# Performance work log

Hardware: AMD Instinct MI355X
Metric: run time of the kernel (lower is better)

Reference implementation:

```python
import jax, jax.numpy as jnp
import numpy as np


def setup_inputs() -> dict:
    key = jax.random.key(0)
    ks = jax.random.split(key, 13)
    T, B, E, H = 2048, 32, 512, 512
    stdv = 1.0 / np.sqrt(H)
    u = lambda k, shape: jax.random.uniform(k, shape, jnp.float32, -stdv, stdv)
    return {
        "embeds": jax.random.normal(ks[0], (T, B, E), jnp.float32),
        "h_0": jnp.zeros((B, H), jnp.float32),
        "c_0": jnp.zeros((B, H), jnp.float32),
        "W_gx": u(ks[1], (E, H)), "W_gh": u(ks[2], (H, H)), "b_g": u(ks[3], (H,)),
        "W_ix": u(ks[4], (E, H)), "W_ih": u(ks[5], (H, H)), "b_i": u(ks[6], (H,)),
        "W_fx": u(ks[7], (E, H)), "W_fh": u(ks[8], (H, H)), "b_f": u(ks[9], (H,)),
        "W_ox": u(ks[10], (E, H)), "W_oh": u(ks[11], (H, H)), "b_o": u(ks[12], (H,)),
    }


def reference(embeds, h_0, c_0, W_gx, W_gh, b_g, W_ix, W_ih, b_i,
              W_fx, W_fh, b_f, W_ox, W_oh, b_o):
    # Fuse the 4 input-side GEMMs into one [T,B,E]@[E,4H] (no recurrence dep).
    Wx = jnp.concatenate([W_gx, W_ix, W_fx, W_ox], axis=1)   # [E, 4H]
    Wh = jnp.concatenate([W_gh, W_ih, W_fh, W_oh], axis=1)   # [H, 4H]
    b = jnp.concatenate([b_g, b_i, b_f, b_o], axis=0)        # [4H]
    H = h_0.shape[-1]
    x_gates = embeds @ Wx + b                                 # [T, B, 4H]

    def step(carry, xg):
        h, c = carry
        gates = xg + h @ Wh                                   # [B, 4H]
        g, i, f, o = jnp.split(gates, 4, axis=-1)
        g = jnp.tanh(g)
        i = jax.nn.sigmoid(i)
        f = jax.nn.sigmoid(f)
        o = jax.nn.sigmoid(o)
        c = g * i + c * f
        h = jnp.tanh(c) * o
        return (h, c), h

    (h_T, c_T), seq = jax.lax.scan(step, (h_0, c_0), x_gates)
    return seq, h_T, c_T
```

## Files before the change

kernel.cpp:

```cpp
#include <hip/hip_runtime.h>


#define T_STEPS 2048
#define BATCH   32
#define EDIM    512
#define HDIM    512
#define NW      128
#define NJ      4
#define NCOL    16
#define WG_THREADS 128
#define BSTRIDE 1032

typedef unsigned int       u32;
typedef unsigned long long u64;
typedef unsigned short     u16;
typedef float  floatx4 __attribute__((ext_vector_type(4)));
typedef __bf16 bf16x8  __attribute__((ext_vector_type(8)));

union BF16U { __bf16 b; u16 u; };

__device__ __forceinline__ u16 f2bf(float f) { BF16U x; x.b = (__bf16)f; return x.u; }

__device__ __forceinline__ float fast_sigmoid(float x) {
  return 1.0f / (1.0f + __expf(-x));
}
__device__ __forceinline__ float fast_tanh(float x) {
  float e = __expf(-2.0f * fabsf(x));
  float t = (1.0f - e) / (1.0f + e);
  return x >= 0.0f ? t : -t;
}

__global__ void lstm_prep(const float* __restrict__ emb, u16* __restrict__ embb,
                          const float* __restrict__ h0, u16* __restrict__ hb0,
                          u32* __restrict__ flags) {
  const size_t n4 = (size_t)T_STEPS * BATCH * EDIM / 4;
  size_t stride = (size_t)gridDim.x * blockDim.x;
  size_t gid = (size_t)blockIdx.x * blockDim.x + threadIdx.x;
  for (size_t i = gid; i < n4; i += stride) {
    float4 v = ((const float4*)emb)[i];
    ushort4 o;
    o.x = f2bf(v.x); o.y = f2bf(v.y); o.z = f2bf(v.z); o.w = f2bf(v.w);
    ((ushort4*)embb)[i] = o;
  }
  if (gid < (size_t)BATCH * HDIM) hb0[gid] = f2bf(h0[gid]);
  if (gid < NW) flags[gid] = 0u;
}

__global__ void __launch_bounds__(WG_THREADS)
lstm_rec(const u16* __restrict__ embb,
         const float* __restrict__ c0,
         const float* __restrict__ Wx0, const float* __restrict__ Wh0, const float* __restrict__ b0,
         const float* __restrict__ Wx1, const float* __restrict__ Wh1, const float* __restrict__ b1,
         const float* __restrict__ Wx2, const float* __restrict__ Wh2, const float* __restrict__ b2,
         const float* __restrict__ Wx3, const float* __restrict__ Wh3, const float* __restrict__ b3,
         u16* __restrict__ hbuf,
         u32* __restrict__ flags,
         float* __restrict__ out) {
  __shared__ __align__(16) __bf16 Blds[NCOL][BSTRIDE];
  __shared__ __align__(16) float wbuf[2][NCOL][20];

  const int tid    = threadIdx.x;
  const int w      = blockIdx.x;
  const int j0     = w * NJ;
  const int lane   = tid & 63;
  const int waveid = tid >> 6;
  const int nlo    = lane & 15;
  const int q      = lane >> 4;
  const int mrow   = waveid * 16 + nlo;

  const float* Wx[4] = {Wx0, Wx1, Wx2, Wx3};
  const float* Wh[4] = {Wh0, Wh1, Wh2, Wh3};

  for (int g = 0; g < 4; ++g) {
    for (int base = 0; base < EDIM; base += WG_THREADS) {
      int kk = base + tid;
      float4 wx = *(const float4*)(Wx[g] + (size_t)kk * HDIM + j0);
      float4 wh = *(const float4*)(Wh[g] + (size_t)kk * HDIM + j0);
      Blds[g*NJ+0][kk] = (__bf16)wx.x;  Blds[g*NJ+0][EDIM+kk] = (__bf16)wh.x;
      Blds[g*NJ+1][kk] = (__bf16)wx.y;  Blds[g*NJ+1][EDIM+kk] = (__bf16)wh.y;
      Blds[g*NJ+2][kk] = (__bf16)wx.z;  Blds[g*NJ+2][EDIM+kk] = (__bf16)wh.z;
      Blds[g*NJ+3][kk] = (__bf16)wx.w;  Blds[g*NJ+3][EDIM+kk] = (__bf16)wh.w;
    }
  }

  const int r0 = nlo >> 2;
  const int ej = nlo & 3;
  const int er = waveid * 16 + q * 4 + r0;
  const int jg = j0 + ej;
  float cst = c0[(size_t)er * HDIM + jg];
  const float bgv = b0[jg], biv = b1[jg], bfv = b2[jg], bov = b3[jg];

  __syncthreads();

  const u64* f8 = (const u64*)flags;

  for (int t = 0; t < T_STEPS; ++t) {
    floatx4 acc0 = {0.f, 0.f, 0.f, 0.f};
    floatx4 acc1 = {0.f, 0.f, 0.f, 0.f};
    const u16* erow = embb + ((size_t)t * BATCH + mrow) * EDIM;
#pragma unroll
    for (int s = 0; s < 16; s += 2) {
      int k0 = s * 32 + q * 8;
      int k1 = (s + 1) * 32 + q * 8;
      bf16x8 a0 = *reinterpret_cast<const bf16x8*>(erow + k0);
      bf16x8 a1 = *reinterpret_cast<const bf16x8*>(erow + k1);
      bf16x8 w0 = *reinterpret_cast<const bf16x8*>(&Blds[nlo][k0]);
      bf16x8 w1 = *reinterpret_cast<const bf16x8*>(&Blds[nlo][k1]);
      acc0 = __builtin_amdgcn_mfma_f32_16x16x32_bf16(a0, w0, acc0, 0, 0, 0);
      acc1 = __builtin_amdgcn_mfma_f32_16x16x32_bf16(a1, w1, acc1, 0, 0, 0);
    }

    for (;;) {
      u64 v = __hip_atomic_load(&f8[lane], __ATOMIC_RELAXED, __HIP_MEMORY_SCOPE_AGENT);
      int ok = ((u32)v >= (u32)t) && ((u32)(v >> 32) >= (u32)t);
      if (__all(ok)) break;
      __builtin_amdgcn_s_sleep(1);
    }

    const u16* hcur  = hbuf + (size_t)(t & 1) * (BATCH * HDIM);
    u16*       hnext = hbuf + (size_t)((t + 1) & 1) * (BATCH * HDIM);

    const u64* hrow = (const u64*)(hcur + (size_t)mrow * HDIM);
#pragma unroll
    for (int s = 0; s < 16; s += 2) {
      int k0 = s * 32 + q * 8;
      int k1 = (s + 1) * 32 + q * 8;
      union { u64 qv[2]; bf16x8 v; } ua, ub;
      ua.qv[0] = __hip_atomic_load(&hrow[(k0 >> 2) + 0], __ATOMIC_RELAXED, __HIP_MEMORY_SCOPE_AGENT);
      ua.qv[1] = __hip_atomic_load(&hrow[(k0 >> 2) + 1], __ATOMIC_RELAXED, __HIP_MEMORY_SCOPE_AGENT);
      ub.qv[0] = __hip_atomic_load(&hrow[(k1 >> 2) + 0], __ATOMIC_RELAXED, __HIP_MEMORY_SCOPE_AGENT);
      ub.qv[1] = __hip_atomic_load(&hrow[(k1 >> 2) + 1], __ATOMIC_RELAXED, __HIP_MEMORY_SCOPE_AGENT);
      bf16x8 w0 = *reinterpret_cast<const bf16x8*>(&Blds[nlo][EDIM + k0]);
      bf16x8 w1 = *reinterpret_cast<const bf16x8*>(&Blds[nlo][EDIM + k1]);
      acc0 = __builtin_amdgcn_mfma_f32_16x16x32_bf16(ua.v, w0, acc0, 0, 0, 0);
      acc1 = __builtin_amdgcn_mfma_f32_16x16x32_bf16(ub.v, w1, acc1, 0, 0, 0);
    }

    floatx4 sum;
#pragma unroll
    for (int r = 0; r < 4; ++r) sum[r] = acc0[r] + acc1[r];
    *reinterpret_cast<floatx4*>(&wbuf[waveid][nlo][q * 4]) = sum;

    float pg = wbuf[waveid][ej     ][q * 4 + r0];
    float pi = wbuf[waveid][ej +  4][q * 4 + r0];
    float pf = wbuf[waveid][ej +  8][q * 4 + r0];
    float po = wbuf[waveid][ej + 12][q * 4 + r0];

    float gv = fast_tanh   (pg + bgv);
    float iv = fast_sigmoid(pi + biv);
    float fv = fast_sigmoid(pf + bfv);
    float ov = fast_sigmoid(po + bov);
    cst = gv * iv + cst * fv;
    float hv = fast_tanh(cst) * ov;

    __hip_atomic_store(hnext + (size_t)er * HDIM + jg, f2bf(hv),
                       __ATOMIC_RELAXED, __HIP_MEMORY_SCOPE_AGENT);
    __syncthreads();
    if (tid == 0)
      __hip_atomic_store(&flags[w], (u32)(t + 1),
                         __ATOMIC_RELAXED, __HIP_MEMORY_SCOPE_AGENT);

    out[((size_t)t * BATCH + er) * HDIM + jg] = hv;
    if (t == T_STEPS - 1) {
      const size_t seqN = (size_t)T_STEPS * BATCH * HDIM;
      out[seqN + (size_t)er * HDIM + jg] = hv;
      out[seqN + (size_t)BATCH * HDIM + (size_t)er * HDIM + jg] = cst;
    }
  }
}

extern "C" void kernel_launch(void* const* d_in, const int* in_sizes, int n_in,
                              void* d_out, int out_size, void* d_ws, size_t ws_size,
                              hipStream_t stream) {
  const float* emb = (const float*)d_in[0];
  const float* h0  = (const float*)d_in[1];
  const float* c0  = (const float*)d_in[2];
  const float* Wgx = (const float*)d_in[3];
  const float* Wgh = (const float*)d_in[4];
  const float* bg  = (const float*)d_in[5];
  const float* Wix = (const float*)d_in[6];
  const float* Wih = (const float*)d_in[7];
  const float* bi  = (const float*)d_in[8];
  const float* Wfx = (const float*)d_in[9];
  const float* Wfh = (const float*)d_in[10];
  const float* bf  = (const float*)d_in[11];
  const float* Wox = (const float*)d_in[12];
  const float* Woh = (const float*)d_in[13];
  const float* bo  = (const float*)d_in[14];
  float* out = (float*)d_out;

  char* ws = (char*)d_ws;
  const size_t embb_bytes = (size_t)T_STEPS * BATCH * EDIM * 2;
  u16* embb  = (u16*)ws;
  u16* hbuf  = (u16*)(ws + embb_bytes);
  u32* flags = (u32*)(ws + embb_bytes + 2 * (size_t)BATCH * HDIM * 2);

  lstm_prep<<<4096, 256, 0, stream>>>(emb, embb, h0, hbuf, flags);
  lstm_rec<<<NW, WG_THREADS, 0, stream>>>(embb, c0,
                                          Wgx, Wgh, bg,
                                          Wix, Wih, bi,
                                          Wfx, Wfh, bf,
                                          Wox, Woh, bo,
                                          hbuf, flags, out);
}
```

Baseline: 7.516 ms.

## Consolidate recurrent LSTM into 32 large workgroups to cut cross-WG sync cost

Reshapes the persistent recurrent kernel from 128 workgroups of 2 waves (4 hidden columns each) into 32 workgroups of 8 waves (16 hidden columns each). Each wave now covers one of 2 batch tiles and one of 4 column tiles. Weights move to dynamic LDS of about 142KB per workgroup. The per-step flag poll only has to check 32 producers, using 16 lanes. The aim is to shrink the per-timestep grid-wide barrier and flag-polling latency. The cost is fewer CUs active and more waves contending for LDS and MFMA units on each CU.

```diff
diff --git a/kernel.cpp b/kernel.cpp
--- a/kernel.cpp
+++ b/kernel.cpp
@@ -5,10 +5,10 @@
 #define BATCH   32
 #define EDIM    512
 #define HDIM    512
-#define NW      128
-#define NJ      4
-#define NCOL    16
-#define WG_THREADS 128
+#define NW      32
+#define NJH     16
+#define NCOL    64
+#define WG_THREADS 512
 #define BSTRIDE 1032
 
 typedef unsigned int       u32;
@@ -16,6 +16,10 @@
 typedef unsigned short     u16;
 typedef float  floatx4 __attribute__((ext_vector_type(4)));
 typedef __bf16 bf16x8  __attribute__((ext_vector_type(8)));
+
+#define BLDS_BYTES (NCOL * BSTRIDE * 2)
+#define WBUF_OFF   BLDS_BYTES
+#define LDS_BYTES  (BLDS_BYTES + 8 * 16 * 20 * 4)
 
 union BF16U { __bf16 b; u16 u; };
 
@@ -56,37 +60,44 @@
          u16* __restrict__ hbuf,
          u32* __restrict__ flags,
          float* __restrict__ out) {
-  __shared__ __align__(16) __bf16 Blds[NCOL][BSTRIDE];
-  __shared__ __align__(16) float wbuf[2][NCOL][20];
+  extern __shared__ __align__(16) char dynlds[];
+  __bf16 (*Blds)[BSTRIDE] = (__bf16(*)[BSTRIDE])dynlds;
+  float  (*wbuf)[16][20]  = (float(*)[16][20])(dynlds + WBUF_OFF);
 
   const int tid    = threadIdx.x;
   const int w      = blockIdx.x;
-  const int j0     = w * NJ;
+  const int j0     = w * NJH;
   const int lane   = tid & 63;
   const int waveid = tid >> 6;
+  const int mtile  = waveid & 1;
+  const int ntile  = waveid >> 1;
   const int nlo    = lane & 15;
   const int q      = lane >> 4;
-  const int mrow   = waveid * 16 + nlo;
+  const int mrow   = mtile * 16 + nlo;
+  const int pbase  = ntile * 16;
 
   const float* Wx[4] = {Wx0, Wx1, Wx2, Wx3};
   const float* Wh[4] = {Wh0, Wh1, Wh2, Wh3};
 
-  for (int g = 0; g < 4; ++g) {
-    for (int base = 0; base < EDIM; base += WG_THREADS) {
-      int kk = base + tid;
-      float4 wx = *(const float4*)(Wx[g] + (size_t)kk * HDIM + j0);
-      float4 wh = *(const float4*)(Wh[g] + (size_t)kk * HDIM + j0);
-      Blds[g*NJ+0][kk] = (__bf16)wx.x;  Blds[g*NJ+0][EDIM+kk] = (__bf16)wh.x;
-      Blds[g*NJ+1][kk] = (__bf16)wx.y;  Blds[g*NJ+1][EDIM+kk] = (__bf16)wh.y;
-      Blds[g*NJ+2][kk] = (__bf16)wx.z;  Blds[g*NJ+2][EDIM+kk] = (__bf16)wh.z;
-      Blds[g*NJ+3][kk] = (__bf16)wx.w;  Blds[g*NJ+3][EDIM+kk] = (__bf16)wh.w;
+  {
+    const int kk = tid;
+    for (int g = 0; g < 4; ++g) {
+      for (int cq = 0; cq < 4; ++cq) {
+        const float4 wxv = *(const float4*)(Wx[g] + (size_t)kk * HDIM + j0 + cq * 4);
+        const float4 whv = *(const float4*)(Wh[g] + (size_t)kk * HDIM + j0 + cq * 4);
+        const int p = cq * 16 + g * 4;
+        Blds[p + 0][kk] = (__bf16)wxv.x;  Blds[p + 0][EDIM + kk] = (__bf16)whv.x;
+        Blds[p + 1][kk] = (__bf16)wxv.y;  Blds[p + 1][EDIM + kk] = (__bf16)whv.y;
+        Blds[p + 2][kk] = (__bf16)wxv.z;  Blds[p + 2][EDIM + kk] = (__bf16)whv.z;
+        Blds[p + 3][kk] = (__bf16)wxv.w;  Blds[p + 3][EDIM + kk] = (__bf16)whv.w;
+      }
     }
   }
 
   const int r0 = nlo >> 2;
   const int ej = nlo & 3;
-  const int er = waveid * 16 + q * 4 + r0;
-  const int jg = j0 + ej;
+  const int er = mtile * 16 + q * 4 + r0;
+  const int jg = j0 + ntile * 4 + ej;
   float cst = c0[(size_t)er * HDIM + jg];
   const float bgv = b0[jg], biv = b1[jg], bfv = b2[jg], bov = b3[jg];
 
@@ -104,15 +115,18 @@
       int k1 = (s + 1) * 32 + q * 8;
       bf16x8 a0 = *reinterpret_cast<const bf16x8*>(erow + k0);
       bf16x8 a1 = *reinterpret_cast<const bf16x8*>(erow + k1);
-      bf16x8 w0 = *reinterpret_cast<const bf16x8*>(&Blds[nlo][k0]);
-      bf16x8 w1 = *reinterpret_cast<const bf16x8*>(&Blds[nlo][k1]);
+      bf16x8 w0 = *reinterpret_cast<const bf16x8*>(&Blds[pbase + nlo][k0]);
+      bf16x8 w1 = *reinterpret_cast<const bf16x8*>(&Blds[pbase + nlo][k1]);
       acc0 = __builtin_amdgcn_mfma_f32_16x16x32_bf16(a0, w0, acc0, 0, 0, 0);
       acc1 = __builtin_amdgcn_mfma_f32_16x16x32_bf16(a1, w1, acc1, 0, 0, 0);
     }
 
     for (;;) {
-      u64 v = __hip_atomic_load(&f8[lane], __ATOMIC_RELAXED, __HIP_MEMORY_SCOPE_AGENT);
-      int ok = ((u32)v >= (u32)t) && ((u32)(v >> 32) >= (u32)t);
+      int ok = 1;
+      if (lane < 16) {
+        u64 v = __hip_atomic_load(&f8[lane], __ATOMIC_RELAXED, __HIP_MEMORY_SCOPE_AGENT);
+        ok = ((u32)v >= (u32)t) && ((u32)(v >> 32) >= (u32)t);
+      }
       if (__all(ok)) break;
       __builtin_amdgcn_s_sleep(1);
     }
@@ -130,8 +144,8 @@
       ua.qv[1] = __hip_atomic_load(&hrow[(k0 >> 2) + 1], __ATOMIC_RELAXED, __HIP_MEMORY_SCOPE_AGENT);
       ub.qv[0] = __hip_atomic_load(&hrow[(k1 >> 2) + 0], __ATOMIC_RELAXED, __HIP_MEMORY_SCOPE_AGENT);
       ub.qv[1] = __hip_atomic_load(&hrow[(k1 >> 2) + 1], __ATOMIC_RELAXED, __HIP_MEMORY_SCOPE_AGENT);
-      bf16x8 w0 = *reinterpret_cast<const bf16x8*>(&Blds[nlo][EDIM + k0]);
-      bf16x8 w1 = *reinterpret_cast<const bf16x8*>(&Blds[nlo][EDIM + k1]);
+      bf16x8 w0 = *reinterpret_cast<const bf16x8*>(&Blds[pbase + nlo][EDIM + k0]);
+      bf16x8 w1 = *reinterpret_cast<const bf16x8*>(&Blds[pbase + nlo][EDIM + k1]);
       acc0 = __builtin_amdgcn_mfma_f32_16x16x32_bf16(ua.v, w0, acc0, 0, 0, 0);
       acc1 = __builtin_amdgcn_mfma_f32_16x16x32_bf16(ub.v, w1, acc1, 0, 0, 0);
     }
@@ -195,11 +209,18 @@
   u16* hbuf  = (u16*)(ws + embb_bytes);
   u32* flags = (u32*)(ws + embb_bytes + 2 * (size_t)BATCH * HDIM * 2);
 
+  static int lds_attr_set = 0;
+  if (!lds_attr_set) {
+    hipFuncSetAttribute(reinterpret_cast<const void*>(lstm_rec),
+                        hipFuncAttributeMaxDynamicSharedMemorySize, LDS_BYTES);
+    lds_attr_set = 1;
+  }
+
   lstm_prep<<<4096, 256, 0, stream>>>(emb, embb, h0, hbuf, flags);
-  lstm_rec<<<NW, WG_THREADS, 0, stream>>>(embb, c0,
-                                          Wgx, Wgh, bg,
-                                          Wix, Wih, bi,
-                                          Wfx, Wfh, bf,
-                                          Wox, Woh, bo,
-                                          hbuf, flags, out);
-}
+  lstm_rec<<<NW, WG_THREADS, LDS_BYTES, stream>>>(embb, c0,
+                                                  Wgx, Wgh, bg,
+                                                  Wix, Wih, bi,
+                                                  Wfx, Wfh, bf,
+                                                  Wox, Woh, bo,
+                                                  hbuf, flags, out);
+}
```

New measurement: 22.86 ms. +204.2%, slower.

## Replace per-block flag barrier with sentinel-tagged triple-buffered hidden state

Applied to the files above, without the earlier changes.

Removes the separate per-workgroup flag array and the __syncthreads plus flag publish each step. Consumers instead spin directly on the hidden-state data, treating a NaN-pattern sentinel as not ready, and reuse the loaded values for the recurrent MFMA. A third h buffer lets each block reset the buffer two steps ahead to the sentinel. Hidden outputs are packed into 64-bit stores, one per row per block, through a small shared-memory transpose. This shortens the critical path between steps, but relies on a real h quad never equalling the sentinel and on the ordering from an explicit vmcnt wait.

```diff
diff --git a/kernel.cpp b/kernel.cpp
--- a/kernel.cpp
+++ b/kernel.cpp
@@ -10,6 +10,7 @@
 #define NCOL    16
 #define WG_THREADS 128
 #define BSTRIDE 1032
+#define HQ      (BATCH * HDIM / 4)
 
 typedef unsigned int       u32;
 typedef unsigned long long u64;
@@ -17,6 +18,8 @@
 typedef float  floatx4 __attribute__((ext_vector_type(4)));
 typedef __bf16 bf16x8  __attribute__((ext_vector_type(8)));
 
+#define SENT64 0x7FC07FC07FC07FC0ULL
+
 union BF16U { __bf16 b; u16 u; };
 
 __device__ __forceinline__ u16 f2bf(float f) { BF16U x; x.b = (__bf16)f; return x.u; }
@@ -31,8 +34,7 @@
 }
 
 __global__ void lstm_prep(const float* __restrict__ emb, u16* __restrict__ embb,
-                          const float* __restrict__ h0, u16* __restrict__ hb0,
-                          u32* __restrict__ flags) {
+                          const float* __restrict__ h0, u16* __restrict__ hb) {
   const size_t n4 = (size_t)T_STEPS * BATCH * EDIM / 4;
   size_t stride = (size_t)gridDim.x * blockDim.x;
   size_t gid = (size_t)blockIdx.x * blockDim.x + threadIdx.x;
@@ -42,8 +44,9 @@
     o.x = f2bf(v.x); o.y = f2bf(v.y); o.z = f2bf(v.z); o.w = f2bf(v.w);
     ((ushort4*)embb)[i] = o;
   }
-  if (gid < (size_t)BATCH * HDIM) hb0[gid] = f2bf(h0[gid]);
-  if (gid < NW) flags[gid] = 0u;
+  if (gid < (size_t)BATCH * HDIM) hb[gid] = f2bf(h0[gid]);
+  u64* hq = (u64*)(hb + (size_t)BATCH * HDIM);
+  if (gid < 2 * HQ) hq[gid] = SENT64;
 }
 
 __global__ void __launch_bounds__(WG_THREADS)
@@ -54,10 +57,10 @@
          const float* __restrict__ Wx2, const float* __restrict__ Wh2, const float* __restrict__ b2,
          const float* __restrict__ Wx3, const float* __restrict__ Wh3, const float* __restrict__ b3,
          u16* __restrict__ hbuf,
-         u32* __restrict__ flags,
          float* __restrict__ out) {
   __shared__ __align__(16) __bf16 Blds[NCOL][BSTRIDE];
   __shared__ __align__(16) float wbuf[2][NCOL][20];
+  __shared__ __align__(16) float pbuf[2][16][4];
 
   const int tid    = threadIdx.x;
   const int w      = blockIdx.x;
@@ -90,9 +93,13 @@
   float cst = c0[(size_t)er * HDIM + jg];
   const float bgv = b0[jg], biv = b1[jg], bfv = b2[jg], bov = b3[jg];
 
+  const bool publane = (lane < 16);
+  const int  pubrow  = waveid * 16 + nlo;
+  const size_t puboff = (((size_t)pubrow * HDIM + j0) >> 2);
+
   __syncthreads();
 
-  const u64* f8 = (const u64*)flags;
+  u64* const hq = (u64*)hbuf;
 
   for (int t = 0; t < T_STEPS; ++t) {
     floatx4 acc0 = {0.f, 0.f, 0.f, 0.f};
@@ -110,26 +117,34 @@
       acc1 = __builtin_amdgcn_mfma_f32_16x16x32_bf16(a1, w1, acc1, 0, 0, 0);
     }
 
+    const u64* hc = hq + (size_t)(t % 3) * HQ;
+    u64*       hn = hq + (size_t)((t + 1) % 3) * HQ;
+    u64*       hs = hq + (size_t)((t + 2) % 3) * HQ;
+
+    const u64* hrow = hc + (size_t)mrow * (HDIM / 4);
+    u64 hreg[32];
     for (;;) {
-      u64 v = __hip_atomic_load(&f8[lane], __ATOMIC_RELAXED, __HIP_MEMORY_SCOPE_AGENT);
-      int ok = ((u32)v >= (u32)t) && ((u32)(v >> 32) >= (u32)t);
+      bool ok = true;
+#pragma unroll
+      for (int i = 0; i < 16; ++i) {
+        int base = i * 8 + q * 2;
+        hreg[2*i]   = __hip_atomic_load(&hrow[base],   __ATOMIC_RELAXED, __HIP_MEMORY_SCOPE_AGENT);
+        hreg[2*i+1] = __hip_atomic_load(&hrow[base+1], __ATOMIC_RELAXED, __HIP_MEMORY_SCOPE_AGENT);
+        ok = ok && (hreg[2*i] != SENT64) && (hreg[2*i+1] != SENT64);
+      }
       if (__all(ok)) break;
-      __builtin_amdgcn_s_sleep(1);
-    }
-
-    const u16* hcur  = hbuf + (size_t)(t & 1) * (BATCH * HDIM);
-    u16*       hnext = hbuf + (size_t)((t + 1) & 1) * (BATCH * HDIM);
-
-    const u64* hrow = (const u64*)(hcur + (size_t)mrow * HDIM);
+    }
+
+    if (publane)
+      __hip_atomic_store(&hs[puboff], SENT64, __ATOMIC_RELAXED, __HIP_MEMORY_SCOPE_AGENT);
+
 #pragma unroll
     for (int s = 0; s < 16; s += 2) {
       int k0 = s * 32 + q * 8;
       int k1 = (s + 1) * 32 + q * 8;
       union { u64 qv[2]; bf16x8 v; } ua, ub;
-      ua.qv[0] = __hip_atomic_load(&hrow[(k0 >> 2) + 0], __ATOMIC_RELAXED, __HIP_MEMORY_SCOPE_AGENT);
-      ua.qv[1] = __hip_atomic_load(&hrow[(k0 >> 2) + 1], __ATOMIC_RELAXED, __HIP_MEMORY_SCOPE_AGENT);
-      ub.qv[0] = __hip_atomic_load(&hrow[(k1 >> 2) + 0], __ATOMIC_RELAXED, __HIP_MEMORY_SCOPE_AGENT);
-      ub.qv[1] = __hip_atomic_load(&hrow[(k1 >> 2) + 1], __ATOMIC_RELAXED, __HIP_MEMORY_SCOPE_AGENT);
+      ua.qv[0] = hreg[2*s];     ua.qv[1] = hreg[2*s+1];
+      ub.qv[0] = hreg[2*s+2];   ub.qv[1] = hreg[2*s+3];
       bf16x8 w0 = *reinterpret_cast<const bf16x8*>(&Blds[nlo][EDIM + k0]);
       bf16x8 w1 = *reinterpret_cast<const bf16x8*>(&Blds[nlo][EDIM + k1]);
       acc0 = __builtin_amdgcn_mfma_f32_16x16x32_bf16(ua.v, w0, acc0, 0, 0, 0);
@@ -153,17 +168,24 @@
     cst = gv * iv + cst * fv;
     float hv = fast_tanh(cst) * ov;
 
-    __hip_atomic_store(hnext + (size_t)er * HDIM + jg, f2bf(hv),
-                       __ATOMIC_RELAXED, __HIP_MEMORY_SCOPE_AGENT);
-    __syncthreads();
-    if (tid == 0)
-      __hip_atomic_store(&flags[w], (u32)(t + 1),
-                         __ATOMIC_RELAXED, __HIP_MEMORY_SCOPE_AGENT);
-
-    out[((size_t)t * BATCH + er) * HDIM + jg] = hv;
+    pbuf[waveid][q * 4 + r0][ej] = hv;
+
+    float4 hv4;
+    if (publane) {
+      floatx4 v4 = *reinterpret_cast<floatx4*>(&pbuf[waveid][nlo][0]);
+      hv4.x = v4[0]; hv4.y = v4[1]; hv4.z = v4[2]; hv4.w = v4[3];
+    }
+    asm volatile("s_waitcnt vmcnt(0)" ::: "memory");
+    if (publane) {
+      u64 pk = (u64)f2bf(hv4.x) | ((u64)f2bf(hv4.y) << 16)
+             | ((u64)f2bf(hv4.z) << 32) | ((u64)f2bf(hv4.w) << 48);
+      __hip_atomic_store(&hn[puboff], pk, __ATOMIC_RELAXED, __HIP_MEMORY_SCOPE_AGENT);
+      *reinterpret_cast<float4*>(out + ((size_t)t * BATCH + pubrow) * HDIM + j0) = hv4;
+    }
     if (t == T_STEPS - 1) {
       const size_t seqN = (size_t)T_STEPS * BATCH * HDIM;
-      out[seqN + (size_t)er * HDIM + jg] = hv;
+      if (publane)
+        *reinterpret_cast<float4*>(out + seqN + (size_t)pubrow * HDIM + j0) = hv4;
       out[seqN + (size_t)BATCH * HDIM + (size_t)er * HDIM + jg] = cst;
     }
   }
@@ -193,13 +215,12 @@
   const size_t embb_bytes = (size_t)T_STEPS * BATCH * EDIM * 2;
   u16* embb  = (u16*)ws;
   u16* hbuf  = (u16*)(ws + embb_bytes);
-  u32* flags = (u32*)(ws + embb_bytes + 2 * (size_t)BATCH * HDIM * 2);
-
-  lstm_prep<<<4096, 256, 0, stream>>>(emb, embb, h0, hbuf, flags);
+
+  lstm_prep<<<4096, 256, 0, stream>>>(emb, embb, h0, hbuf);
   lstm_rec<<<NW, WG_THREADS, 0, stream>>>(embb, c0,
                                           Wgx, Wgh, bg,
                                           Wix, Wih, bi,
                                           Wfx, Wfh, bf,
                                           Wox, Woh, bo,
-                                          hbuf, flags, out);
-}
+                                          hbuf, out);
+}
```

Result: slower. 10.75 ms (+43.0%).

## Use per-wave flags, packed h stores, and prefetch embeddings into registers

Applied to the files above, without the earlier changes.

Splits the step-completion flags so each wave publishes and waits on its own set, which removes the per-step block-wide __syncthreads. Each group of four lanes packs its bf16 h values into one 64-bit atomic store and writes the fp32 output as a float4. The next step's embedding rows are prefetched into registers while the current step runs, and the sleep in the spin loop is removed. The costs are higher register pressure, busier spinning on the flags, and reliance on a raw s_waitcnt to order the h store before the flag store.

```diff
diff --git a/kernel.cpp b/kernel.cpp
--- a/kernel.cpp
+++ b/kernel.cpp
@@ -31,7 +31,7 @@
 }
 
 __global__ void lstm_prep(const float* __restrict__ emb, u16* __restrict__ embb,
-                          const float* __restrict__ h0, u16* __restrict__ hb0,
+                          const float* __restrict__ h0, u16* __restrict__ hb,
                           u32* __restrict__ flags) {
   const size_t n4 = (size_t)T_STEPS * BATCH * EDIM / 4;
   size_t stride = (size_t)gridDim.x * blockDim.x;
@@ -42,8 +42,8 @@
     o.x = f2bf(v.x); o.y = f2bf(v.y); o.z = f2bf(v.z); o.w = f2bf(v.w);
     ((ushort4*)embb)[i] = o;
   }
-  if (gid < (size_t)BATCH * HDIM) hb0[gid] = f2bf(h0[gid]);
-  if (gid < NW) flags[gid] = 0u;
+  if (gid < (size_t)BATCH * HDIM) hb[gid] = f2bf(h0[gid]);
+  if (gid < 2 * NW) flags[gid] = 0u;
 }
 
 __global__ void __launch_bounds__(WG_THREADS)
@@ -90,35 +90,50 @@
   float cst = c0[(size_t)er * HDIM + jg];
   const float bgv = b0[jg], biv = b1[jg], bfv = b2[jg], bov = b3[jg];
 
+  const bool publane = (ej == 0);
+  const size_t puboff = (size_t)er * (HDIM / 4) + w;
+
   __syncthreads();
 
-  const u64* f8 = (const u64*)flags;
+  const u64* f8 = (const u64*)(flags + waveid * NW);
+  u32* const myflag = flags + waveid * NW + w;
+
+  bf16x8 ereg[16];
+  {
+    const u16* erow = embb + (size_t)mrow * EDIM;
+#pragma unroll
+    for (int s = 0; s < 16; ++s)
+      ereg[s] = *reinterpret_cast<const bf16x8*>(erow + s * 32 + q * 8);
+  }
 
   for (int t = 0; t < T_STEPS; ++t) {
     floatx4 acc0 = {0.f, 0.f, 0.f, 0.f};
     floatx4 acc1 = {0.f, 0.f, 0.f, 0.f};
-    const u16* erow = embb + ((size_t)t * BATCH + mrow) * EDIM;
 #pragma unroll
     for (int s = 0; s < 16; s += 2) {
       int k0 = s * 32 + q * 8;
       int k1 = (s + 1) * 32 + q * 8;
-      bf16x8 a0 = *reinterpret_cast<const bf16x8*>(erow + k0);
-      bf16x8 a1 = *reinterpret_cast<const bf16x8*>(erow + k1);
       bf16x8 w0 = *reinterpret_cast<const bf16x8*>(&Blds[nlo][k0]);
       bf16x8 w1 = *reinterpret_cast<const bf16x8*>(&Blds[nlo][k1]);
-      acc0 = __builtin_amdgcn_mfma_f32_16x16x32_bf16(a0, w0, acc0, 0, 0, 0);
-      acc1 = __builtin_amdgcn_mfma_f32_16x16x32_bf16(a1, w1, acc1, 0, 0, 0);
+      acc0 = __builtin_amdgcn_mfma_f32_16x16x32_bf16(ereg[s],     w0, acc0, 0, 0, 0);
+      acc1 = __builtin_amdgcn_mfma_f32_16x16x32_bf16(ereg[s + 1], w1, acc1, 0, 0, 0);
+    }
+
+    if (t + 1 < T_STEPS) {
+      const u16* erow = embb + ((size_t)(t + 1) * BATCH + mrow) * EDIM;
+#pragma unroll
+      for (int s = 0; s < 16; ++s)
+        ereg[s] = *reinterpret_cast<const bf16x8*>(erow + s * 32 + q * 8);
     }
 
     for (;;) {
       u64 v = __hip_atomic_load(&f8[lane], __ATOMIC_RELAXED, __HIP_MEMORY_SCOPE_AGENT);
       int ok = ((u32)v >= (u32)t) && ((u32)(v >> 32) >= (u32)t);
       if (__all(ok)) break;
-      __builtin_amdgcn_s_sleep(1);
     }
 
     const u16* hcur  = hbuf + (size_t)(t & 1) * (BATCH * HDIM);
-    u16*       hnext = hbuf + (size_t)((t + 1) & 1) * (BATCH * HDIM);
+    u64*       hnext = (u64*)(hbuf + (size_t)((t + 1) & 1) * (BATCH * HDIM));
 
     const u64* hrow = (const u64*)(hcur + (size_t)mrow * HDIM);
 #pragma unroll
@@ -153,17 +168,30 @@
     cst = gv * iv + cst * fv;
     float hv = fast_tanh(cst) * ov;
 
-    __hip_atomic_store(hnext + (size_t)er * HDIM + jg, f2bf(hv),
-                       __ATOMIC_RELAXED, __HIP_MEMORY_SCOPE_AGENT);
-    __syncthreads();
-    if (tid == 0)
-      __hip_atomic_store(&flags[w], (u32)(t + 1),
-                         __ATOMIC_RELAXED, __HIP_MEMORY_SCOPE_AGENT);
-
-    out[((size_t)t * BATCH + er) * HDIM + jg] = hv;
+    u32 b16  = (u32)f2bf(hv);
+    u32 lo32 = b16 | (((u32)__shfl_xor((int)b16, 1)) << 16);
+    u32 hi32 = (u32)__shfl_xor((int)lo32, 2);
+    u64 pk   = (u64)lo32 | ((u64)hi32 << 32);
+
+    if (publane)
+      __hip_atomic_store(&hnext[puboff], pk, __ATOMIC_RELAXED, __HIP_MEMORY_SCOPE_AGENT);
+    asm volatile("s_waitcnt vmcnt(0)" ::: "memory");
+    if (lane == 0)
+      __hip_atomic_store(myflag, (u32)(t + 1), __ATOMIC_RELAXED, __HIP_MEMORY_SCOPE_AGENT);
+
+    float f1 = __shfl_xor(hv, 1);
+    float f2 = __shfl_xor(hv, 2);
+    float f3 = __shfl_xor(f1, 2);
+    if (publane) {
+      float4 hv4 = {hv, f1, f2, f3};
+      *reinterpret_cast<float4*>(out + ((size_t)t * BATCH + er) * HDIM + j0) = hv4;
+      if (t == T_STEPS - 1) {
+        const size_t seqN = (size_t)T_STEPS * BATCH * HDIM;
+        *reinterpret_cast<float4*>(out + seqN + (size_t)er * HDIM + j0) = hv4;
+      }
+    }
     if (t == T_STEPS - 1) {
       const size_t seqN = (size_t)T_STEPS * BATCH * HDIM;
-      out[seqN + (size_t)er * HDIM + jg] = hv;
       out[seqN + (size_t)BATCH * HDIM + (size_t)er * HDIM + jg] = cst;
     }
   }
```

Result: slower. 8.804 ms (+17.1%).
